# Kernel tuning notes

Measured on AMD Instinct MI355X. Metric: run time of the kernel, lower is better.

## Reference

```python
import jax, jax.numpy as jnp
import numpy as np

EPS = 1e-5

def conv3x3(x, w, b=None):
    # NCHW, OIHW, stride 1, padding 1
    y = jax.lax.conv_general_dilated(x, w, (1, 1), ((1, 1), (1, 1)),
                                     dimension_numbers=('NCHW', 'OIHW', 'NCHW'))
    if b is not None:
        y = y + b[None, :, None, None]
    return y

def batchnorm(x, g, b):
    # training-mode BN (PyTorch default): biased variance over (N,H,W)
    m = x.mean((0, 2, 3), keepdims=True)
    v = x.var((0, 2, 3), keepdims=True)
    return (x - m) * jax.lax.rsqrt(v + EPS) * g[None, :, None, None] + b[None, :, None, None]

def upsample2x_align_corners(x):
    # bilinear, align_corners=True, scale_factor=2
    def lerp_axis(a, Lin, axis):
        Lout = 2 * Lin
        c = jnp.arange(Lout, dtype=a.dtype) * (Lin - 1) / (Lout - 1)
        i0 = jnp.floor(c).astype(jnp.int32)
        i1 = jnp.minimum(i0 + 1, Lin - 1)
        w = c - i0.astype(a.dtype)
        shape = [1] * a.ndim
        shape[axis] = Lout
        w = w.reshape(shape)
        return jnp.take(a, i0, axis=axis) * (1 - w) + jnp.take(a, i1, axis=axis) * w
    x = lerp_axis(x, x.shape[2], 2)
    x = lerp_axis(x, x.shape[3], 3)
    return x

def deform_sample(x, offsets):
    # torchvision DeformConv2d v1 sampling: kernel 3x3, pad 1, offsets [B,18,H,W]
    # layout: per kernel point k (row-major), channels (2k, 2k+1) = (dy, dx)
    B, C, H, W = x.shape
    K = 9
    off = offsets.reshape(B, K, 2, H, W)
    ky, kx = jnp.meshgrid(jnp.arange(3) - 1, jnp.arange(3) - 1, indexing='ij')
    ky = ky.reshape(K).astype(x.dtype)
    kx = kx.reshape(K).astype(x.dtype)
    gy = jnp.arange(H, dtype=x.dtype)[None, None, :, None]
    gx = jnp.arange(W, dtype=x.dtype)[None, None, None, :]
    py = gy + ky[None, :, None, None] + off[:, :, 0]  # [B,K,H,W]
    px = gx + kx[None, :, None, None] + off[:, :, 1]
    y0 = jnp.floor(py)
    x0 = jnp.floor(px)
    wy = (py - y0)[:, None]  # [B,1,K,H,W]
    wx = (px - x0)[:, None]
    y0i = y0.astype(jnp.int32)
    x0i = x0.astype(jnp.int32)
    x_flat = x.reshape(B, C, H * W)
    def gather(yi, xi):
        valid = ((yi >= 0) & (yi < H) & (xi >= 0) & (xi < W))
        idx = jnp.clip(yi, 0, H - 1) * W + jnp.clip(xi, 0, W - 1)  # [B,K,H,W]
        g = jnp.take_along_axis(x_flat, idx.reshape(B, 1, K * H * W), axis=2)
        return g.reshape(B, C, K, H, W) * valid[:, None].astype(x.dtype)
    v00 = gather(y0i, x0i)
    v01 = gather(y0i, x0i + 1)
    v10 = gather(y0i + 1, x0i)
    v11 = gather(y0i + 1, x0i + 1)
    return (v00 * (1 - wy) * (1 - wx) + v01 * (1 - wy) * wx
            + v10 * wy * (1 - wx) + v11 * wy * wx)

def setup_inputs() -> dict:
    key = jax.random.key(0)
    ks = jax.random.split(key, 6)
    B, in_ch, skip_ch, out_ch = 4, 256, 128, 128
    Hs, Ws = 128, 128
    x = jax.random.normal(ks[0], (B, in_ch, Hs // 2, Ws // 2), jnp.float32)
    skip = jax.random.normal(ks[1], (B, skip_ch, Hs, Ws), jnp.float32)
    cat_ch = in_ch + skip_ch
    conv1_w = jax.random.normal(ks[2], (out_ch, cat_ch, 3, 3), jnp.float32) * (2.0 / (cat_ch * 9)) ** 0.5
    off_w = jax.random.normal(ks[3], (18, out_ch, 3, 3), jnp.float32) * 0.01
    off_b = jnp.zeros((18,), jnp.float32)
    def_w = jax.random.normal(ks[4], (out_ch, out_ch, 3, 3), jnp.float32) * (2.0 / (out_ch * 9)) ** 0.5
    def_b = jnp.zeros((out_ch,), jnp.float32)
    return {
        'x': x, 'skip': skip,
        'conv1_w': conv1_w,
        'bn1_g': jnp.ones((out_ch,), jnp.float32), 'bn1_b': jnp.zeros((out_ch,), jnp.float32),
        'off_w': off_w, 'off_b': off_b,
        'def_w': def_w, 'def_b': def_b,
        'bn2_g': jnp.ones((out_ch,), jnp.float32), 'bn2_b': jnp.zeros((out_ch,), jnp.float32),
    }

def reference(x, skip, conv1_w, bn1_g, bn1_b, off_w, off_b, def_w, def_b, bn2_g, bn2_b):
    xu = upsample2x_align_corners(x)
    dh = skip.shape[2] - xu.shape[2]
    dw = skip.shape[3] - xu.shape[3]
    if dh != 0 or dw != 0:
        xu = jnp.pad(xu, ((0, 0), (0, 0), (dh // 2, dh - dh // 2), (dw // 2, dw - dw // 2)))
    cat = jnp.concatenate([skip, xu], axis=1)
    h = jax.nn.relu(batchnorm(conv3x3(cat, conv1_w), bn1_g, bn1_b))
    offsets = conv3x3(h, off_w, off_b)  # [B,18,H,W]
    sampled = deform_sample(h, offsets)  # [B,C,9,H,W]
    O = def_w.shape[0]
    y = jnp.einsum('ock,bckhw->bohw', def_w.reshape(O, def_w.shape[1], 9), sampled)
    y = y + def_b[None, :, None, None]
    return jax.nn.relu(batchnorm(y, bn2_g, bn2_b))
```

## Files before the change

### kernel.cpp

```cpp
#include <hip/hip_runtime.h>
#include <hip/hip_bf16.h>

typedef __hip_bfloat16 bf16;
typedef __bf16 bf16x8 __attribute__((ext_vector_type(8)));
typedef __bf16 bf16x4 __attribute__((ext_vector_type(4)));
typedef float  f32x4  __attribute__((ext_vector_type(4)));

constexpr int NB   = 4;
constexpr int H    = 128;
constexpr int W    = 128;
constexpr int HW   = H * W;
constexpr int NPIX = NB * HW;
constexpr int CCAT = 384;
constexpr int CSKIP= 128;
constexpr int CIN  = 256;
constexpr int CO   = 128;
constexpr int HS   = 64;
constexpr int WP   = 130;
constexpr int K1   = 3456;
constexpr int KD   = 1152;
constexpr int NBORD= 2 * WP + 2 * (WP - 2);
constexpr float EPS = 1e-5f;

constexpr int NTR  = CO * K1 + 32 * KD + CO * KD;
constexpr int NCATB= NB * NBORD * CCAT;
constexpr int NHPB = NB * NBORD * CO;

__device__ __forceinline__ float b2f(bf16 v){ return __bfloat162float(v); }
__device__ __forceinline__ bf16  f2b(float v){ return __float2bfloat16(v); }

__device__ __forceinline__ void async_copy16(const void* g, void* s){
    __builtin_amdgcn_global_load_lds((const __attribute__((address_space(1))) void*)g,
                                     (__attribute__((address_space(3))) void*)s, 16, 0, 0);
}

__device__ __forceinline__ void border_yx(int p, int& y, int& x){
    if (p < WP)             { y = 0;        x = p; }
    else if (p < 2 * WP)    { y = WP - 1;   x = p - WP; }
    else if (p < 2 * WP + (WP - 2)) { y = p - 2 * WP + 1;          x = 0; }
    else                    { y = p - (2 * WP + (WP - 2)) + 1;     x = WP - 1; }
}

__global__ __launch_bounds__(256) void k_setup(const float* __restrict__ x,
                                               const float* __restrict__ skip,
                                               const float* __restrict__ w1,
                                               const float* __restrict__ wo,
                                               const float* __restrict__ wd,
                                               float* __restrict__ sums,
                                               bf16* __restrict__ catp,
                                               bf16* __restrict__ hp,
                                               bf16* __restrict__ wt1,
                                               bf16* __restrict__ wto,
                                               bf16* __restrict__ wtd){
    constexpr int TS = 66;
    __shared__ bf16 tile[128 * TS];
    int t = threadIdx.x;

    if (blockIdx.x < NB * H){
        int y  = blockIdx.x % H, b = blockIdx.x / H;
        int xx = t & 127, cp = t >> 7;

        float cy = (y * 63.0f) / 127.0f;
        int   y0 = (int)cy;
        int   y1 = min(y0 + 1, HS - 1);
        float wy = cy - y0;
        float cxf = (xx * 63.0f) / 127.0f;
        int   x0 = (int)cxf;
        int   x1 = min(x0 + 1, HS - 1);
        float wx = cxf - x0;

        bf16* orow = catp + (((size_t)b * WP + y + 1) * WP + 1) * CCAT;

        for (int chunk = 0; chunk < 6; chunk++){
            int cbase = chunk * 64;
            if (chunk >= 1) __syncthreads();
            if (chunk < 2){
                const float* sb = skip + ((size_t)(b * CSKIP + cbase + cp * 32) * H + y) * W;
#pragma unroll
                for (int i = 0; i < 32; i++)
                    tile[xx * TS + cp * 32 + i] = f2b(sb[(size_t)i * HW + xx]);
            } else {
                int icb = (chunk - 2) * 64 + cp * 32;
                const float* xr0 = x + ((size_t)(b * CIN + icb) * HS + y0) * HS;
                const float* xr1 = x + ((size_t)(b * CIN + icb) * HS + y1) * HS;
#pragma unroll
                for (int i = 0; i < 32; i++){
                    const float* r0 = xr0 + (size_t)i * HS * HS;
                    const float* r1 = xr1 + (size_t)i * HS * HS;
                    float v0 = r0[x0] * (1 - wx) + r0[x1] * wx;
                    float v1 = r1[x0] * (1 - wx) + r1[x1] * wx;
                    tile[xx * TS + cp * 32 + i] = f2b(v0 * (1 - wy) + v1 * wy);
                }
            }
            __syncthreads();
            int cc2 = (t & 31) * 2;
            int px0 = t >> 5;
#pragma unroll
            for (int pp = 0; pp < 16; pp++){
                int px = pp * 8 + px0;
                unsigned int v = *(const unsigned int*)&tile[px * TS + cc2];
                *(unsigned int*)&orow[(size_t)px * CCAT + cbase + cc2] = v;
            }
        }
        return;
    }

    int idx = (blockIdx.x - NB * H) * 256 + t;
    if (idx < NTR){
        int i = idx;
        if (i < CO * K1){
            int e  = i & 7;
            int l  = (i >> 3) & 63;
            int nb = (i >> 9) & 7;
            int ks = (i >> 12) & 1;
            int p  = i >> 13;
            int gp = p / 6, q = p - gp * 6;
            int ky = gp / 3, ci = gp - ky * 3;
            int kx = q >> 1, s64 = q & 1;
            int oc = nb * 16 + (l & 15);
            int ic = ci * 128 + s64 * 64 + ks * 32 + (l >> 4) * 8 + e;
            wt1[i] = f2b(w1[((oc * CCAT + ic) * 3 + ky) * 3 + kx]);
            return;
        }
        i -= CO * K1;
        if (i < 32 * KD){
            int e  = i & 7;
            int l  = (i >> 3) & 63;
            int wn = (i >> 9) & 1;
            int s  = (i >> 10) & 3;
            int kk = i >> 12;
            int ky = kk / 3, kx = kk - ky * 3;
            int oc = wn * 16 + (l & 15);
            int ic = s * 32 + (l >> 4) * 8 + e;
            wto[i] = (oc < 18) ? f2b(wo[((oc * CO + ic) * 3 + ky) * 3 + kx]) : f2b(0.f);
            return;
        }
        i -= 32 * KD;
        int e  = i & 7;
        int l  = (i >> 3) & 63;
        int ni = (i >> 9) & 3;
        int wn = (i >> 11) & 1;
        int ks = (i >> 12) & 1;
        int kc = i >> 13;
        int oc = wn * 64 + ni * 16 + (l & 15);
        int ic = (kc & 1) * 64 + ks * 32 + (l >> 4) * 8 + e;
        int kp = kc >> 1;
        wtd[i] = f2b(wd[(oc * CO + ic) * 9 + kp]);
        return;
    }
    idx -= NTR;
    if (idx < 512){ sums[idx] = 0.f; return; }
    idx -= 512;
    if (idx < NCATB){
        int c = idx % CCAT, r = idx / CCAT, p = r % NBORD, b = r / NBORD;
        int y, xw; border_yx(p, y, xw);
        catp[(((size_t)b * WP + y) * WP + xw) * CCAT + c] = f2b(0.f);
        return;
    }
    idx -= NCATB;
    if (idx < NHPB){
        int c = idx % CO, r = idx / CO, p = r % NBORD, b = r / NBORD;
        int y, xw; border_yx(p, y, xw);
        hp[(((size_t)b * WP + y) * WP + xw) * CO + c] = f2b(0.f);
    }
}

__global__ __launch_bounds__(256) void k_conv1_mfma(const bf16* __restrict__ catp,
                                                    const bf16* __restrict__ wbt,
                                                    bf16* __restrict__ hp,
                                                    float* __restrict__ sums){
    __shared__ unsigned short Ab[2][68 * 128];
    __shared__ float ps[256];
    int t = threadIdx.x;
    int l = t & 63, w = t >> 6;
    int half = blockIdx.x & 1;
    int y = (blockIdx.x >> 1) % H, b = blockIdx.x / (2 * H);
    int px0 = half * 64;

    int m = l & 15, quad = l >> 4;

    f32x4 acc[4][2];
#pragma unroll
    for (int i = 0; i < 4; i++)
#pragma unroll
        for (int j = 0; j < 2; j++) acc[i][j] = f32x4{0.f, 0.f, 0.f, 0.f};

    const size_t rowStride = (size_t)WP * CCAT;
    const char* wq = (const char*)wbt + w * 2048 + l * 16;

    bf16x8 bA[2][2], bB[2][2];

    {
        const bf16* Arow = catp + ((size_t)(b * WP) + y) * rowStride + (size_t)px0 * CCAT;
        for (int i = w; i < 17; i += 4){
            int G = i * 64 + l;
            int px = G >> 4, ol = G & 15;
            int osrc = ol ^ (px & 15);
            async_copy16(Arow + (size_t)px * CCAT + osrc * 8, &Ab[0][i * 512]);
        }
#pragma unroll
        for (int ks = 0; ks < 2; ks++)
#pragma unroll
            for (int ni = 0; ni < 2; ni++)
                bA[ks][ni] = *(const bf16x8*)(wq + ks * 8192 + ni * 1024);
    }
    __syncthreads();

#pragma unroll 1
    for (int g = 0; g < 9; g++){
        if (g < 8){
            int gn = g + 1;
            int kyn = gn / 3, cin = gn - kyn * 3;
            const bf16* Arow = catp + ((size_t)(b * WP) + y + kyn) * rowStride
                             + (size_t)px0 * CCAT + cin * 128;
            for (int i = w; i < 17; i += 4){
                int G = i * 64 + l;
                int px = G >> 4, ol = G & 15;
                int osrc = ol ^ (px & 15);
                async_copy16(Arow + (size_t)px * CCAT + osrc * 8, &Ab[gn & 1][i * 512]);
            }
        }
        const bf16x8* ap = (const bf16x8*)&Ab[g & 1][0];
        const char* wg = wq + (size_t)g * 6 * 16384;
#pragma unroll
        for (int j = 0; j < 6; j++){
            int kx = j >> 1, s64 = j & 1;
            const char* wnx = wg + (j + 1) * 16384;
            if (j & 1){
#pragma unroll
                for (int ks = 0; ks < 2; ks++)
#pragma unroll
                    for (int ni = 0; ni < 2; ni++)
                        bA[ks][ni] = *(const bf16x8*)(wnx + ks * 8192 + ni * 1024);
            } else {
#pragma unroll
                for (int ks = 0; ks < 2; ks++)
#pragma unroll
                    for (int ni = 0; ni < 2; ni++)
                        bB[ks][ni] = *(const bf16x8*)(wnx + ks * 8192 + ni * 1024);
            }
#pragma unroll
            for (int ks = 0; ks < 2; ks++){
                int s = s64 * 2 + ks;
                bf16x8 af[4];
#pragma unroll
                for (int mi = 0; mi < 4; mi++){
                    int pxk = mi * 16 + m + kx;
                    af[mi] = ap[pxk * 16 + ((s * 4 + quad) ^ (pxk & 15))];
                }
                if (j & 1){
#pragma unroll
                    for (int mi = 0; mi < 4; mi++)
#pragma unroll
                        for (int ni = 0; ni < 2; ni++)
                            acc[mi][ni] = __builtin_amdgcn_mfma_f32_16x16x32_bf16(
                                af[mi], bB[ks][ni], acc[mi][ni], 0, 0, 0);
                } else {
#pragma unroll
                    for (int mi = 0; mi < 4; mi++)
#pragma unroll
                        for (int ni = 0; ni < 2; ni++)
                            acc[mi][ni] = __builtin_amdgcn_mfma_f32_16x16x32_bf16(
                                af[mi], bA[ks][ni], acc[mi][ni], 0, 0, 0);
                }
            }
        }
        __syncthreads();
    }

    size_t obase = (((size_t)b * WP + y + 1) * WP + 1 + px0) * CO;
#pragma unroll
    for (int mi = 0; mi < 4; mi++){
        int p0 = mi * 16 + quad * 4;
#pragma unroll
        for (int ni = 0; ni < 2; ni++){
            int oc = w * 32 + ni * 16 + m;
#pragma unroll
            for (int r = 0; r < 4; r++)
                hp[obase + (size_t)(p0 + r) * CO + oc] = f2b(acc[mi][ni][r]);
        }
    }
    ps[t] = 0.f;
    __syncthreads();
#pragma unroll
    for (int ni = 0; ni < 2; ni++){
        int ch = w * 32 + ni * 16 + m;
        float s = 0.f, q2 = 0.f;
#pragma unroll
        for (int mi = 0; mi < 4; mi++)
#pragma unroll
            for (int r = 0; r < 4; r++){
                float v = acc[mi][ni][r];
                s += v; q2 += v * v;
            }
        s += __shfl_xor(s, 16); s += __shfl_xor(s, 32);
        q2 += __shfl_xor(q2, 16); q2 += __shfl_xor(q2, 32);
        if (quad == 0){
            atomicAdd(&ps[ch], s);
            atomicAdd(&ps[128 + ch], q2);
        }
    }
    __syncthreads();
    if (t < 128){
        atomicAdd(&sums[t],       ps[t]);
        atomicAdd(&sums[128 + t], ps[128 + t]);
    }
}

__global__ __launch_bounds__(256) void k_conv_off_mfma(const bf16* __restrict__ hp,
                                                       const bf16* __restrict__ wob,
                                                       const float* __restrict__ off_b,
                                                       const float* __restrict__ sums,
                                                       const float* __restrict__ bn_g,
                                                       const float* __restrict__ bn_b,
                                                       bf16* __restrict__ offs,
                                                       bf16* __restrict__ hq){
    __shared__ unsigned short Ab[68 * 128];
    __shared__ float2 ssc[128];
    int t = threadIdx.x, l = t & 63, w = t >> 6;
    if (t < 128){
        float mean = sums[t] / (float)NPIX;
        float var  = sums[128 + t] / (float)NPIX - mean * mean;
        float sc   = bn_g[t] * rsqrtf(var + EPS);
        ssc[t] = make_float2(sc, bn_b[t] - mean * sc);
    }
    int half = blockIdx.x & 1;
    int y = (blockIdx.x >> 1) % H, b = blockIdx.x / (2 * H);
    int px0 = half * 64;
    int m = l & 15, quad = l >> 4;
    int wm = w & 1, wn = w >> 1;

    f32x4 acc[2];
#pragma unroll
    for (int i = 0; i < 2; i++) acc[i] = f32x4{0.f, 0.f, 0.f, 0.f};

    const size_t rowStrideH = (size_t)WP * CO;
    const char* wq = (const char*)wob + wn * 1024 + l * 16;
    __syncthreads();

    for (int ky = 0; ky < 3; ky++){
        if (ky) __syncthreads();
        int row = y + ky;
        const bf16* Arow = hp + ((size_t)(b * WP) + row) * rowStrideH
                         + (size_t)px0 * CO;
        bool rowborder = (row == 0) || (row == WP - 1);
        bf16* hqrow = hq + ((size_t)(b * WP) + row) * rowStrideH;
        for (int i = w; i < 17; i += 4){
            int G  = i * 64 + l;
            int px = G >> 4, ol = G & 15;
            int osrc = ol ^ (px & 15);
            int col = px0 + px;
            bool zero = rowborder || (col == 0) || (col >= WP - 1);
            bf16x8 raw = *(const bf16x8*)(Arow + (size_t)px * CO + osrc * 8);
            bf16x8 outv;
#pragma unroll
            for (int e = 0; e < 8; e++){
                float2 sb = ssc[osrc * 8 + e];
                float v = (float)raw[e] * sb.x + sb.y;
                v = v > 0.f ? v : 0.f;
                outv[e] = zero ? (__bf16)0.f : (__bf16)v;
            }
            *(bf16x8*)&Ab[G * 8] = outv;
            if (ky == 1 && col >= 1 && col <= 128)
                *(bf16x8*)(hqrow + (size_t)col * CO + osrc * 8) = outv;
        }
        bf16x8 bfr[3][4];
#pragma unroll
        for (int kx = 0; kx < 3; kx++)
#pragma unroll
            for (int s = 0; s < 4; s++)
                bfr[kx][s] = *(const bf16x8*)(wq + (((ky * 3 + kx) * 4 + s) * 2048));
        __syncthreads();
        const bf16x8* ap = (const bf16x8*)Ab;
        for (int kx = 0; kx < 3; kx++){
#pragma unroll
            for (int s = 0; s < 4; s++){
#pragma unroll
                for (int mi = 0; mi < 2; mi++){
                    int pxk = wm * 32 + mi * 16 + m + kx;
                    bf16x8 af = ap[pxk * 16 + ((s * 4 + quad) ^ (pxk & 15))];
                    acc[mi] = __builtin_amdgcn_mfma_f32_16x16x32_bf16(af, bfr[kx][s], acc[mi], 0, 0, 0);
                }
            }
        }
    }
    int oc = wn * 16 + m;
    if (oc < 18){
        float bias = off_b[oc];
        int rowpix = b * HW + y * W + px0;
#pragma unroll
        for (int mi = 0; mi < 2; mi++){
            int p0 = wm * 32 + mi * 16 + quad * 4;
#pragma unroll
            for (int r = 0; r < 4; r++)
                offs[(size_t)(rowpix + p0 + r) * 18 + oc] = f2b(acc[mi][r] + bias);
        }
    }
}

__global__ __launch_bounds__(256) void k_deform_mfma(const bf16* __restrict__ hq,
                                                     const bf16* __restrict__ offs,
                                                     const bf16* __restrict__ wdb,
                                                     const float* __restrict__ def_b,
                                                     bf16* __restrict__ y,
                                                     float* __restrict__ sums){
    __shared__ unsigned short Ab[2][128 * 64];
    __shared__ int2   sc_yx[9 * 128];
    __shared__ float4 sc_w[9 * 128];
    __shared__ float  ps[256];

    int t = threadIdx.x, l = t & 63, w = t >> 6;
    int yrow = blockIdx.x % H, b = blockIdx.x / H;
    int rowpix = b * HW + yrow * W;

    for (int idx = t; idx < 9 * 128; idx += 256){
        int kp = idx >> 7, px = idx & 127;
        float dy = b2f(offs[(size_t)(rowpix + px) * 18 + 2 * kp]);
        float dx = b2f(offs[(size_t)(rowpix + px) * 18 + 2 * kp + 1]);
        float py = yrow + (kp / 3 - 1) + dy;
        float pxx = px + (kp % 3 - 1) + dx;
        float fy = floorf(py), fx = floorf(pxx);
        float wy = py - fy, wx = pxx - fx;
        int y0 = (int)fy, x0 = (int)fx;
        bool vy0 = (y0 >= 0) && (y0 < H);
        bool vy1 = (y0 + 1 >= 0) && (y0 + 1 < H);
        bool vx0 = (x0 >= 0) && (x0 < W);
        bool vx1 = (x0 + 1 >= 0) && (x0 + 1 < W);
        int y0c = min(max(y0, 0), H - 1),     y1c = min(max(y0 + 1, 0), H - 1);
        int x0c = min(max(x0, 0), W - 1),     x1c = min(max(x0 + 1, 0), W - 1);
        sc_yx[idx] = make_int2(((y0c + 1) * WP) | (((y1c + 1) * WP) << 16),
                               (x0c + 1) | ((x1c + 1) << 16));
        sc_w[idx] = make_float4((1 - wy) * (1 - wx) * (float)(vy0 && vx0),
                                (1 - wy) * wx       * (float)(vy0 && vx1),
                                wy * (1 - wx)       * (float)(vy1 && vx0),
                                wy * wx             * (float)(vy1 && vx1));
    }
    __syncthreads();

    int m = l & 15, quad = l >> 4;
    int wm = w & 1, wn = w >> 1;
    int g = l >> 4, j = l & 15;

    f32x4 acc[4][4];
#pragma unroll
    for (int i = 0; i < 4; i++)
#pragma unroll
        for (int jj = 0; jj < 4; jj++) acc[i][jj] = f32x4{0.f, 0.f, 0.f, 0.f};

    const bf16* hpb = hq + (size_t)b * WP * WP * CO;
    const char* wq = (const char*)wdb + wn * 4096 + l * 16;

    auto GEN = [&](int kc, unsigned short* dst){
        int kp = kc >> 1, ch = (kc & 1) * 64;
        int cb = ch + j * 4;
#pragma unroll
        for (int p = 0; p < 8; p++){
            int px = w * 32 + g * 8 + p;
            int idx = kp * 128 + px;
            int2 yx = sc_yx[idx];
            float4 w4 = sc_w[idx];
            int r0 = yx.x & 0xffff, r1 = ((unsigned)yx.x) >> 16;
            int c0 = yx.y & 0xffff, c1 = ((unsigned)yx.y) >> 16;
            const bf16* base = hpb + cb;
            bf16x4 s00 = *(const bf16x4*)(base + (size_t)(r0 + c0) * CO);
            bf16x4 s01 = *(const bf16x4*)(base + (size_t)(r0 + c1) * CO);
            bf16x4 s10 = *(const bf16x4*)(base + (size_t)(r1 + c0) * CO);
            bf16x4 s11 = *(const bf16x4*)(base + (size_t)(r1 + c1) * CO);
            bf16x4 pv;
#pragma unroll
            for (int r = 0; r < 4; r++){
                float v = w4.x * (float)s00[r] + w4.y * (float)s01[r]
                        + w4.z * (float)s10[r] + w4.w * (float)s11[r];
                pv[r] = (__bf16)v;
            }
            int oct_sw = (j >> 1) ^ (px & 7);
            *(bf16x4*)&dst[px * 64 + oct_sw * 8 + (j & 1) * 4] = pv;
        }
    };

    GEN(0, &Ab[0][0]);

#pragma unroll 1
    for (int kc = 0; kc < 18; kc++){
        __syncthreads();
        bf16x8 bfr[2][4];
        const char* wk = wq + (size_t)kc * 16384;
#pragma unroll
        for (int ks = 0; ks < 2; ks++)
#pragma unroll
            for (int ni = 0; ni < 4; ni++)
                bfr[ks][ni] = *(const bf16x8*)(wk + ks * 8192 + ni * 1024);
        if (kc < 17) GEN(kc + 1, &Ab[(kc + 1) & 1][0]);

        const bf16x8* ap = (const bf16x8*)&Ab[kc & 1][0];
#pragma unroll
        for (int ks = 0; ks < 2; ks++){
            bf16x8 af[4];
#pragma unroll
            for (int mi = 0; mi < 4; mi++){
                int px = wm * 64 + mi * 16 + m;
                af[mi] = ap[px * 8 + ((ks * 4 + quad) ^ (px & 7))];
            }
#pragma unroll
            for (int mi = 0; mi < 4; mi++)
#pragma unroll
                for (int ni = 0; ni < 4; ni++)
                    acc[mi][ni] = __builtin_amdgcn_mfma_f32_16x16x32_bf16(
                        af[mi], bfr[ks][ni], acc[mi][ni], 0, 0, 0);
        }
    }
#pragma unroll
    for (int mi = 0; mi < 4; mi++){
        int p0 = wm * 64 + mi * 16 + quad * 4;
#pragma unroll
        for (int ni = 0; ni < 4; ni++){
            int oc = wn * 64 + ni * 16 + m;
            float bias = def_b[oc];
#pragma unroll
            for (int r = 0; r < 4; r++)
                y[(size_t)(rowpix + p0 + r) * CO + oc] = f2b(acc[mi][ni][r] + bias);
        }
    }
    ps[t] = 0.f;
    __syncthreads();
#pragma unroll
    for (int ni = 0; ni < 4; ni++){
        int ch = wn * 64 + ni * 16 + m;
        float bias = def_b[ch];
        float s = 0.f, q = 0.f;
#pragma unroll
        for (int mi = 0; mi < 4; mi++)
#pragma unroll
            for (int r = 0; r < 4; r++){
                float v = acc[mi][ni][r] + bias;
                s += v; q += v * v;
            }
        s += __shfl_xor(s, 16); s += __shfl_xor(s, 32);
        q += __shfl_xor(q, 16); q += __shfl_xor(q, 32);
        if (quad == 0){
            atomicAdd(&ps[ch], s);
            atomicAdd(&ps[128 + ch], q);
        }
    }
    __syncthreads();
    if (t < 128){
        atomicAdd(&sums[t],       ps[t]);
        atomicAdd(&sums[128 + t], ps[128 + t]);
    }
}

__global__ __launch_bounds__(256) void k_final(const bf16* __restrict__ yb,
                                               const float* __restrict__ sums,
                                               const float* __restrict__ g,
                                               const float* __restrict__ bb,
                                               float* __restrict__ out){
    __shared__ unsigned short tile[128 * 129];
    __shared__ float ssc[256];
    int t = threadIdx.x;
    if (t < 128){
        float mean = sums[t] / (float)NPIX;
        float var  = sums[128 + t] / (float)NPIX - mean * mean;
        float scale = g[t] * rsqrtf(var + EPS);
        ssc[t]       = scale;
        ssc[128 + t] = bb[t] - mean * scale;
    }
    int yrow = blockIdx.x % H, b = blockIdx.x / H;
    int rowbase = b * HW + yrow * W;
    const unsigned short* src = (const unsigned short*)yb;
    for (int it = 0; it < 64; it++){
        int idx = it * 256 + t;
        int c = idx & 127, px = idx >> 7;
        tile[px * 129 + c] = src[(size_t)(rowbase + px) * CO + c];
    }
    __syncthreads();
    for (int it = 0; it < 64; it++){
        int idx = it * 256 + t;
        int xw = idx & 127, o = idx >> 7;
        unsigned short u = tile[xw * 129 + o];
        float v = (float)(*(const __bf16*)&u);
        v = v * ssc[o] + ssc[128 + o];
        out[(((size_t)b * CO + o) * H + yrow) * W + xw] = v > 0.f ? v : 0.f;
    }
}

extern "C" void kernel_launch(void* const* d_in, const int* in_sizes, int n_in,
                              void* d_out, int out_size, void* d_ws, size_t ws_size,
                              hipStream_t stream){
    const float* x      = (const float*)d_in[0];
    const float* skip   = (const float*)d_in[1];
    const float* conv1w = (const float*)d_in[2];
    const float* bn1g   = (const float*)d_in[3];
    const float* bn1b   = (const float*)d_in[4];
    const float* offw   = (const float*)d_in[5];
    const float* offb   = (const float*)d_in[6];
    const float* defw   = (const float*)d_in[7];
    const float* defb   = (const float*)d_in[8];
    const float* bn2g   = (const float*)d_in[9];
    const float* bn2b   = (const float*)d_in[10];
    float* out = (float*)d_out;

    char* ws = (char*)d_ws;
    size_t off_bytes = 0;
    auto alloc = [&](size_t bytes) -> void* {
        void* p = ws + off_bytes;
        off_bytes += (bytes + 255) & ~(size_t)255;
        return p;
    };
    const size_t catp_elems = (size_t)NB * WP * WP * CCAT;
    const size_t hp_elems   = (size_t)NB * WP * WP * CO;
    bf16*  catp  = (bf16*) alloc(catp_elems * 2 + 2048);
    bf16*  hp    = (bf16*) alloc(hp_elems * 2 + 2048);
    bf16*  hq    = (bf16*) alloc(hp_elems * 2 + 2048);
    bf16*  offs  = (bf16*) alloc((size_t)NPIX * 18 * 2);
    bf16*  yb    = (bf16*) alloc((size_t)NPIX * CO * 2);
    bf16*  wbt   = (bf16*) alloc((size_t)CO * K1 * 2 + 32768);
    bf16*  wob   = (bf16*) alloc((size_t)32 * KD * 2);
    bf16*  wdb   = (bf16*) alloc((size_t)CO * KD * 2);
    float* sums  = (float*)alloc(512 * 4);
    float* sums1 = sums;
    float* sums2 = sums + 256;

    const int nflat = NTR + 512 + NCATB + NHPB;
    const int setup_blocks = NB * H + (nflat + 255) / 256;

    k_setup<<<setup_blocks, 256, 0, stream>>>(x, skip, conv1w, offw, defw,
                                              sums, catp, hp, wbt, wob, wdb);

    k_conv1_mfma<<<NB * H * 2, 256, 0, stream>>>(catp, wbt, hp, sums1);

    k_conv_off_mfma<<<NB * H * 2, 256, 0, stream>>>(hp, wob, offb, sums1,
                                                    bn1g, bn1b, offs, hq);

    k_deform_mfma<<<NB * H, 256, 0, stream>>>(hq, offs, wdb, defb, yb, sums2);

    k_final<<<NB * H, 256, 0, stream>>>(yb, sums2, bn2g, bn2b, out);
}
```

Baseline: 314.5 us.

## Fuse all stages into one persistent kernel with software grid barriers

Replaces the five separate kernel launches (setup, conv1, offset conv, deformable conv, final BN) with a single persistent kernel of 256 blocks that grid-strides over row tiles and separates the stages with atomic-counter grid barriers. The aim is to remove per-launch overhead and the idle gaps between dependent kernels. In exchange the grid is limited to 256 blocks with launch bounds of 1, which lowers occupancy and the parallelism of the MFMA stages. Correctness also depends on every block being co-resident and on the spin barrier behaving correctly.

```diff
diff --git a/kernel.cpp b/kernel.cpp
--- a/kernel.cpp
+++ b/kernel.cpp
@@ -25,6 +25,9 @@
 constexpr int NTR  = CO * K1 + 32 * KD + CO * KD;
 constexpr int NCATB= NB * NBORD * CCAT;
 constexpr int NHPB = NB * NBORD * CO;
+constexpr int NFLAT= NTR + 512 + NCATB + NHPB;
+
+constexpr int GRID = 256;
 
 __device__ __forceinline__ float b2f(bf16 v){ return __bfloat162float(v); }
 __device__ __forceinline__ bf16  f2b(float v){ return __float2bfloat16(v); }
@@ -41,33 +44,49 @@
     else                    { y = p - (2 * WP + (WP - 2)) + 1;     x = WP - 1; }
 }
 
-__global__ __launch_bounds__(256) void k_setup(const float* __restrict__ x,
-                                               const float* __restrict__ skip,
-                                               const float* __restrict__ w1,
-                                               const float* __restrict__ wo,
-                                               const float* __restrict__ wd,
-                                               float* __restrict__ sums,
-                                               bf16* __restrict__ catp,
-                                               bf16* __restrict__ hp,
-                                               bf16* __restrict__ wt1,
-                                               bf16* __restrict__ wto,
-                                               bf16* __restrict__ wtd){
-    constexpr int TS = 66;
-    __shared__ bf16 tile[128 * TS];
+__device__ __forceinline__ void gsync(unsigned* bar, unsigned target){
+    __syncthreads();
+    if (threadIdx.x == 0){
+        __threadfence();
+        atomicAdd(bar, 1u);
+        while (atomicAdd(bar, 0u) < target)
+            __builtin_amdgcn_s_sleep(8);
+        __threadfence();
+    }
+    __syncthreads();
+}
+
+__global__ void __launch_bounds__(256, 1) k_fused(
+    const float* __restrict__ x,    const float* __restrict__ skip,
+    const float* __restrict__ w1,   const float* __restrict__ bn1g,
+    const float* __restrict__ bn1b, const float* __restrict__ wo,
+    const float* __restrict__ offb, const float* __restrict__ wd,
+    const float* __restrict__ defb, const float* __restrict__ bn2g,
+    const float* __restrict__ bn2b, float* __restrict__ out,
+    bf16* __restrict__ catp, bf16* __restrict__ hp, bf16* __restrict__ hq,
+    bf16* __restrict__ offs, bf16* __restrict__ yb,
+    bf16* __restrict__ wt1, bf16* __restrict__ wto, bf16* __restrict__ wtd,
+    float* __restrict__ sums, unsigned* __restrict__ bar)
+{
+    __shared__ __align__(16) char smem[61440];
     int t = threadIdx.x;
-
-    if (blockIdx.x < NB * H){
-        int y  = blockIdx.x % H, b = blockIdx.x / H;
+    float* sums1 = sums;
+    float* sums2 = sums + 256;
+
+    for (int vb = blockIdx.x; vb < 512; vb += GRID){
+        constexpr int TS = 66;
+        bf16* tile = (bf16*)smem;
+        int y  = vb % H, b = vb / H;
         int xx = t & 127, cp = t >> 7;
 
         float cy = (y * 63.0f) / 127.0f;
         int   y0 = (int)cy;
         int   y1 = min(y0 + 1, HS - 1);
-        float wy = cy - y0;
+        float wyf = cy - y0;
         float cxf = (xx * 63.0f) / 127.0f;
         int   x0 = (int)cxf;
         int   x1 = min(x0 + 1, HS - 1);
-        float wx = cxf - x0;
+        float wxf = cxf - x0;
 
         bf16* orow = catp + (((size_t)b * WP + y + 1) * WP + 1) * CCAT;
 
@@ -87,9 +106,9 @@
                 for (int i = 0; i < 32; i++){
                     const float* r0 = xr0 + (size_t)i * HS * HS;
                     const float* r1 = xr1 + (size_t)i * HS * HS;
-                    float v0 = r0[x0] * (1 - wx) + r0[x1] * wx;
-                    float v1 = r1[x0] * (1 - wx) + r1[x1] * wx;
-                    tile[xx * TS + cp * 32 + i] = f2b(v0 * (1 - wy) + v1 * wy);
+                    float v0 = r0[x0] * (1 - wxf) + r0[x1] * wxf;
+                    float v1 = r1[x0] * (1 - wxf) + r1[x1] * wxf;
+                    tile[xx * TS + cp * 32 + i] = f2b(v0 * (1 - wyf) + v1 * wyf);
                 }
             }
             __syncthreads();
@@ -102,11 +121,9 @@
                 *(unsigned int*)&orow[(size_t)px * CCAT + cbase + cc2] = v;
             }
         }
-        return;
+        __syncthreads();
     }
-
-    int idx = (blockIdx.x - NB * H) * 256 + t;
-    if (idx < NTR){
+    for (int idx = blockIdx.x * 256 + t; idx < NFLAT; idx += GRID * 256){
         int i = idx;
         if (i < CO * K1){
             int e  = i & 7;
@@ -120,7 +137,7 @@
             int oc = nb * 16 + (l & 15);
             int ic = ci * 128 + s64 * 64 + ks * 32 + (l >> 4) * 8 + e;
             wt1[i] = f2b(w1[((oc * CCAT + ic) * 3 + ky) * 3 + kx]);
-            return;
+            continue;
         }
         i -= CO * K1;
         if (i < 32 * KD){
@@ -133,453 +150,446 @@
             int oc = wn * 16 + (l & 15);
             int ic = s * 32 + (l >> 4) * 8 + e;
             wto[i] = (oc < 18) ? f2b(wo[((oc * CO + ic) * 3 + ky) * 3 + kx]) : f2b(0.f);
-            return;
+            continue;
         }
         i -= 32 * KD;
-        int e  = i & 7;
-        int l  = (i >> 3) & 63;
-        int ni = (i >> 9) & 3;
-        int wn = (i >> 11) & 1;
-        int ks = (i >> 12) & 1;
-        int kc = i >> 13;
-        int oc = wn * 64 + ni * 16 + (l & 15);
-        int ic = (kc & 1) * 64 + ks * 32 + (l >> 4) * 8 + e;
-        int kp = kc >> 1;
-        wtd[i] = f2b(wd[(oc * CO + ic) * 9 + kp]);
-        return;
+        if (i < CO * KD){
+            int e  = i & 7;
+            int l  = (i >> 3) & 63;
+            int ni = (i >> 9) & 3;
+            int wn = (i >> 11) & 1;
+            int ks = (i >> 12) & 1;
+            int kc = i >> 13;
+            int oc = wn * 64 + ni * 16 + (l & 15);
+            int ic = (kc & 1) * 64 + ks * 32 + (l >> 4) * 8 + e;
+            int kp = kc >> 1;
+            wtd[i] = f2b(wd[(oc * CO + ic) * 9 + kp]);
+            continue;
+        }
+        i -= CO * KD;
+        if (i < 512){ sums[i] = 0.f; continue; }
+        i -= 512;
+        if (i < NCATB){
+            int c = i % CCAT, r = i / CCAT, p = r % NBORD, b2 = r / NBORD;
+            int yy, xw; border_yx(p, yy, xw);
+            catp[(((size_t)b2 * WP + yy) * WP + xw) * CCAT + c] = f2b(0.f);
+            continue;
+        }
+        i -= NCATB;
+        {
+            int c = i % CO, r = i / CO, p = r % NBORD, b2 = r / NBORD;
+            int yy, xw; border_yx(p, yy, xw);
+            hp[(((size_t)b2 * WP + yy) * WP + xw) * CO + c] = f2b(0.f);
+        }
     }
-    idx -= NTR;
-    if (idx < 512){ sums[idx] = 0.f; return; }
-    idx -= 512;
-    if (idx < NCATB){
-        int c = idx % CCAT, r = idx / CCAT, p = r % NBORD, b = r / NBORD;
-        int y, xw; border_yx(p, y, xw);
-        catp[(((size_t)b * WP + y) * WP + xw) * CCAT + c] = f2b(0.f);
-        return;
+    gsync(bar, GRID * 1);
+
+    for (int vb = blockIdx.x; vb < 512; vb += GRID){
+        typedef unsigned short AbT[68 * 128];
+        AbT* Ab = (AbT*)smem;
+        float* ps = (float*)(smem + 34816);
+        int l = t & 63, w = t >> 6;
+        int y = vb % H, b = vb / H;
+        int m = l & 15, quad = l >> 4;
+        const size_t rowStride = (size_t)WP * CCAT;
+        const char* wq = (const char*)wt1 + w * 2048 + l * 16;
+
+        for (int u = 0; u < 2; u++){
+            int px0 = u * 64;
+            f32x4 acc[4][2];
+#pragma unroll
+            for (int i = 0; i < 4; i++)
+#pragma unroll
+                for (int j = 0; j < 2; j++) acc[i][j] = f32x4{0.f, 0.f, 0.f, 0.f};
+
+            bf16x8 bA[2][2], bB[2][2];
+            {
+                const bf16* Arow = catp + ((size_t)(b * WP) + y) * rowStride + (size_t)px0 * CCAT;
+                for (int i = w; i < 17; i += 4){
+                    int G = i * 64 + l;
+                    int px = G >> 4, ol = G & 15;
+                    int osrc = ol ^ (px & 15);
+                    async_copy16(Arow + (size_t)px * CCAT + osrc * 8, &Ab[0][i * 512]);
+                }
+#pragma unroll
+                for (int ks = 0; ks < 2; ks++)
+#pragma unroll
+                    for (int ni = 0; ni < 2; ni++)
+                        bA[ks][ni] = *(const bf16x8*)(wq + ks * 8192 + ni * 1024);
+            }
+            __syncthreads();
+
+#pragma unroll 1
+            for (int g = 0; g < 9; g++){
+                if (g < 8){
+                    int gn = g + 1;
+                    int kyn = gn / 3, cin = gn - kyn * 3;
+                    const bf16* Arow = catp + ((size_t)(b * WP) + y + kyn) * rowStride
+                                     + (size_t)px0 * CCAT + cin * 128;
+                    for (int i = w; i < 17; i += 4){
+                        int G = i * 64 + l;
+                        int px = G >> 4, ol = G & 15;
+                        int osrc = ol ^ (px & 15);
+                        async_copy16(Arow + (size_t)px * CCAT + osrc * 8, &Ab[gn & 1][i * 512]);
+                    }
+                }
+                const bf16x8* ap = (const bf16x8*)&Ab[g & 1][0];
+                const char* wg = wq + (size_t)g * 6 * 16384;
+#pragma unroll
+                for (int j = 0; j < 6; j++){
+                    int kx = j >> 1, s64 = j & 1;
+                    const char* wnx = wg + (j + 1) * 16384;
+                    if (j & 1){
+#pragma unroll
+                        for (int ks = 0; ks < 2; ks++)
+#pragma unroll
+                            for (int ni = 0; ni < 2; ni++)
+                                bA[ks][ni] = *(const bf16x8*)(wnx + ks * 8192 + ni * 1024);
+                    } else {
+#pragma unroll
+                        for (int ks = 0; ks < 2; ks++)
+#pragma unroll
+                            for (int ni = 0; ni < 2; ni++)
+                                bB[ks][ni] = *(const bf16x8*)(wnx + ks * 8192 + ni * 1024);
+                    }
+#pragma unroll
+                    for (int ks = 0; ks < 2; ks++){
+                        int s = s64 * 2 + ks;
+                        bf16x8 af[4];
+#pragma unroll
+                        for (int mi = 0; mi < 4; mi++){
+                            int pxk = mi * 16 + m + kx;
+                            af[mi] = ap[pxk * 16 + ((s * 4 + quad) ^ (pxk & 15))];
+                        }
+                        if (j & 1){
+#pragma unroll
+                            for (int mi = 0; mi < 4; mi++)
+#pragma unroll
+                                for (int ni = 0; ni < 2; ni++)
+                                    acc[mi][ni] = __builtin_amdgcn_mfma_f32_16x16x32_bf16(
+                                        af[mi], bB[ks][ni], acc[mi][ni], 0, 0, 0);
+                        } else {
+#pragma unroll
+                            for (int mi = 0; mi < 4; mi++)
+#pragma unroll
+                                for (int ni = 0; ni < 2; ni++)
+                                    acc[mi][ni] = __builtin_amdgcn_mfma_f32_16x16x32_bf16(
+                                        af[mi], bA[ks][ni], acc[mi][ni], 0, 0, 0);
+                        }
+                    }
+                }
+                __syncthreads();
+            }
+
+            size_t obase = (((size_t)b * WP + y + 1) * WP + 1 + px0) * CO;
+#pragma unroll
+            for (int mi = 0; mi < 4; mi++){
+                int p0 = mi * 16 + quad * 4;
+#pragma unroll
+                for (int ni = 0; ni < 2; ni++){
+                    int oc = w * 32 + ni * 16 + m;
+#pragma unroll
+                    for (int r = 0; r < 4; r++)
+                        hp[obase + (size_t)(p0 + r) * CO + oc] = f2b(acc[mi][ni][r]);
+                }
+            }
+            ps[t] = 0.f;
+            __syncthreads();
+#pragma unroll
+            for (int ni = 0; ni < 2; ni++){
+                int ch = w * 32 + ni * 16 + m;
+                float s = 0.f, q2 = 0.f;
+#pragma unroll
+                for (int mi = 0; mi < 4; mi++)
+#pragma unroll
+                    for (int r = 0; r < 4; r++){
+                        float v = acc[mi][ni][r];
+                        s += v; q2 += v * v;
+                    }
+                s += __shfl_xor(s, 16); s += __shfl_xor(s, 32);
+                q2 += __shfl_xor(q2, 16); q2 += __shfl_xor(q2, 32);
+                if (quad == 0){
+                    atomicAdd(&ps[ch], s);
+                    atomicAdd(&ps[128 + ch], q2);
+                }
+            }
+            __syncthreads();
+            if (t < 128){
+                atomicAdd(&sums1[t],       ps[t]);
+                atomicAdd(&sums1[128 + t], ps[128 + t]);
+            }
+            __syncthreads();
+        }
     }
-    idx -= NCATB;
-    if (idx < NHPB){
-        int c = idx % CO, r = idx / CO, p = r % NBORD, b = r / NBORD;
-        int y, xw; border_yx(p, y, xw);
-        hp[(((size_t)b * WP + y) * WP + xw) * CO + c] = f2b(0.f);
+    gsync(bar, GRID * 2);
+
+    {
+        unsigned short* Ab = (unsigned short*)smem;
+        float2* ssc = (float2*)(smem + 17408);
+        int l = t & 63, w = t >> 6;
+        if (t < 128){
+            float mean = sums1[t] / (float)NPIX;
+            float var  = sums1[128 + t] / (float)NPIX - mean * mean;
+            float sc   = bn1g[t] * rsqrtf(var + EPS);
+            ssc[t] = make_float2(sc, bn1b[t] - mean * sc);
+        }
+        int m = l & 15, quad = l >> 4;
+        int wm = w & 1, wn = w >> 1;
+        const size_t rowStrideH = (size_t)WP * CO;
+        const char* wq = (const char*)wto + wn * 1024 + l * 16;
+        __syncthreads();
+
+        for (int vb = blockIdx.x; vb < 512; vb += GRID){
+            int y = vb % H, b = vb / H;
+            for (int u = 0; u < 2; u++){
+                int px0 = u * 64;
+                f32x4 acc[2];
+#pragma unroll
+                for (int i = 0; i < 2; i++) acc[i] = f32x4{0.f, 0.f, 0.f, 0.f};
+
+                for (int ky = 0; ky < 3; ky++){
+                    __syncthreads();
+                    int row = y + ky;
+                    const bf16* Arow = hp + ((size_t)(b * WP) + row) * rowStrideH
+                                     + (size_t)px0 * CO;
+                    bool rowborder = (row == 0) || (row == WP - 1);
+                    bf16* hqrow = hq + ((size_t)(b * WP) + row) * rowStrideH;
+                    for (int i = w; i < 17; i += 4){
+                        int G  = i * 64 + l;
+                        int px = G >> 4, ol = G & 15;
+                        int osrc = ol ^ (px & 15);
+                        int col = px0 + px;
+                        bool zero = rowborder || (col == 0) || (col >= WP - 1);
+                        bf16x8 raw = *(const bf16x8*)(Arow + (size_t)px * CO + osrc * 8);
+                        bf16x8 outv;
+#pragma unroll
+                        for (int e = 0; e < 8; e++){
+                            float2 sb = ssc[osrc * 8 + e];
+                            float v = (float)raw[e] * sb.x + sb.y;
+                            v = v > 0.f ? v : 0.f;
+                            outv[e] = zero ? (__bf16)0.f : (__bf16)v;
+                        }
+                        *(bf16x8*)&Ab[G * 8] = outv;
+                        if (ky == 1 && col >= 1 && col <= 128)
+                            *(bf16x8*)(hqrow + (size_t)col * CO + osrc * 8) = outv;
+                    }
+                    bf16x8 bfr[3][4];
+#pragma unroll
+                    for (int kx = 0; kx < 3; kx++)
+#pragma unroll
+                        for (int s = 0; s < 4; s++)
+                            bfr[kx][s] = *(const bf16x8*)(wq + (((ky * 3 + kx) * 4 + s) * 2048));
+                    __syncthreads();
+                    const bf16x8* ap = (const bf16x8*)Ab;
+                    for (int kx = 0; kx < 3; kx++){
+#pragma unroll
+                        for (int s = 0; s < 4; s++){
+#pragma unroll
+                            for (int mi = 0; mi < 2; mi++){
+                                int pxk = wm * 32 + mi * 16 + m + kx;
+                                bf16x8 af = ap[pxk * 16 + ((s * 4 + quad) ^ (pxk & 15))];
+                                acc[mi] = __builtin_amdgcn_mfma_f32_16x16x32_bf16(af, bfr[kx][s], acc[mi], 0, 0, 0);
+                            }
+                        }
+                    }
+                }
+                int oc = wn * 16 + m;
+                if (oc < 18){
+                    float bias = offb[oc];
+                    int rowpix = b * HW + y * W + px0;
+#pragma unroll
+                    for (int mi = 0; mi < 2; mi++){
+                        int p0 = wm * 32 + mi * 16 + quad * 4;
+#pragma unroll
+                        for (int r = 0; r < 4; r++)
+                            offs[(size_t)(rowpix + p0 + r) * 18 + oc] = f2b(acc[mi][r] + bias);
+                    }
+                }
+                __syncthreads();
+            }
+        }
     }
-}
-
-__global__ __launch_bounds__(256) void k_conv1_mfma(const bf16* __restrict__ catp,
-                                                    const bf16* __restrict__ wbt,
-                                                    bf16* __restrict__ hp,
-                                                    float* __restrict__ sums){
-    __shared__ unsigned short Ab[2][68 * 128];
-    __shared__ float ps[256];
-    int t = threadIdx.x;
-    int l = t & 63, w = t >> 6;
-    int half = blockIdx.x & 1;
-    int y = (blockIdx.x >> 1) % H, b = blockIdx.x / (2 * H);
-    int px0 = half * 64;
-
-    int m = l & 15, quad = l >> 4;
-
-    f32x4 acc[4][2];
-#pragma unroll
-    for (int i = 0; i < 4; i++)
-#pragma unroll
-        for (int j = 0; j < 2; j++) acc[i][j] = f32x4{0.f, 0.f, 0.f, 0.f};
-
-    const size_t rowStride = (size_t)WP * CCAT;
-    const char* wq = (const char*)wbt + w * 2048 + l * 16;
-
-    bf16x8 bA[2][2], bB[2][2];
-
-    {
-        const bf16* Arow = catp + ((size_t)(b * WP) + y) * rowStride + (size_t)px0 * CCAT;
-        for (int i = w; i < 17; i += 4){
-            int G = i * 64 + l;
-            int px = G >> 4, ol = G & 15;
-            int osrc = ol ^ (px & 15);
-            async_copy16(Arow + (size_t)px * CCAT + osrc * 8, &Ab[0][i * 512]);
-        }
-#pragma unroll
-        for (int ks = 0; ks < 2; ks++)
-#pragma unroll
-            for (int ni = 0; ni < 2; ni++)
-                bA[ks][ni] = *(const bf16x8*)(wq + ks * 8192 + ni * 1024);
-    }
-    __syncthreads();
+    gsync(bar, GRID * 3);
+
+    for (int vb = blockIdx.x; vb < 512; vb += GRID){
+        typedef unsigned short AbT[128 * 64];
+        AbT* Ab = (AbT*)smem;
+        int2*   sc_yx = (int2*)(smem + 32768);
+        float4* sc_w  = (float4*)(smem + 41984);
+        float*  ps    = (float*)(smem + 60416);
+        int l = t & 63, w = t >> 6;
+        int yrow = vb % H, b = vb / H;
+        int rowpix = b * HW + yrow * W;
+
+        for (int idx = t; idx < 9 * 128; idx += 256){
+            int kp = idx >> 7, px = idx & 127;
+            float dy = b2f(offs[(size_t)(rowpix + px) * 18 + 2 * kp]);
+            float dx = b2f(offs[(size_t)(rowpix + px) * 18 + 2 * kp + 1]);
+            float py = yrow + (kp / 3 - 1) + dy;
+            float pxx = px + (kp % 3 - 1) + dx;
+            float fy = floorf(py), fx = floorf(pxx);
+            float wy = py - fy, wx = pxx - fx;
+            int y0 = (int)fy, x0 = (int)fx;
+            bool vy0 = (y0 >= 0) && (y0 < H);
+            bool vy1 = (y0 + 1 >= 0) && (y0 + 1 < H);
+            bool vx0 = (x0 >= 0) && (x0 < W);
+            bool vx1 = (x0 + 1 >= 0) && (x0 + 1 < W);
+            int y0c = min(max(y0, 0), H - 1),     y1c = min(max(y0 + 1, 0), H - 1);
+            int x0c = min(max(x0, 0), W - 1),     x1c = min(max(x0 + 1, 0), W - 1);
+            sc_yx[idx] = make_int2(((y0c + 1) * WP) | (((y1c + 1) * WP) << 16),
+                                   (x0c + 1) | ((x1c + 1) << 16));
+            sc_w[idx] = make_float4((1 - wy) * (1 - wx) * (float)(vy0 && vx0),
+                                    (1 - wy) * wx       * (float)(vy0 && vx1),
+                                    wy * (1 - wx)       * (float)(vy1 && vx0),
+                                    wy * wx             * (float)(vy1 && vx1));
+        }
+        __syncthreads();
+
+        int m = l & 15, quad = l >> 4;
+        int wm = w & 1, wn = w >> 1;
+        int g = l >> 4, j = l & 15;
+
+        f32x4 acc[4][4];
+#pragma unroll
+        for (int i = 0; i < 4; i++)
+#pragma unroll
+            for (int jj = 0; jj < 4; jj++) acc[i][jj] = f32x4{0.f, 0.f, 0.f, 0.f};
+
+        const bf16* hpb = hq + (size_t)b * WP * WP * CO;
+        const char* wq = (const char*)wtd + wn * 4096 + l * 16;
+
+        auto GEN = [&](int kc, unsigned short* dst){
+            int kp = kc >> 1, ch = (kc & 1) * 64;
+            int cb = ch + j * 4;
+#pragma unroll
+            for (int p = 0; p < 8; p++){
+                int px = w * 32 + g * 8 + p;
+                int idx = kp * 128 + px;
+                int2 yx = sc_yx[idx];
+                float4 w4 = sc_w[idx];
+                int r0 = yx.x & 0xffff, r1 = ((unsigned)yx.x) >> 16;
+                int c0 = yx.y & 0xffff, c1 = ((unsigned)yx.y) >> 16;
+                const bf16* base = hpb + cb;
+                bf16x4 s00 = *(const bf16x4*)(base + (size_t)(r0 + c0) * CO);
+                bf16x4 s01 = *(const bf16x4*)(base + (size_t)(r0 + c1) * CO);
+                bf16x4 s10 = *(const bf16x4*)(base + (size_t)(r1 + c0) * CO);
+                bf16x4 s11 = *(const bf16x4*)(base + (size_t)(r1 + c1) * CO);
+                bf16x4 pv;
+#pragma unroll
+                for (int r = 0; r < 4; r++){
+                    float v = w4.x * (float)s00[r] + w4.y * (float)s01[r]
+                            + w4.z * (float)s10[r] + w4.w * (float)s11[r];
+                    pv[r] = (__bf16)v;
+                }
+                int oct_sw = (j >> 1) ^ (px & 7);
+                *(bf16x4*)&dst[px * 64 + oct_sw * 8 + (j & 1) * 4] = pv;
+            }
+        };
+
+        GEN(0, &Ab[0][0]);
 
 #pragma unroll 1
-    for (int g = 0; g < 9; g++){
-        if (g < 8){
-            int gn = g + 1;
-            int kyn = gn / 3, cin = gn - kyn * 3;
-            const bf16* Arow = catp + ((size_t)(b * WP) + y + kyn) * rowStride
-                             + (size_t)px0 * CCAT + cin * 128;
-            for (int i = w; i < 17; i += 4){
-                int G = i * 64 + l;
-                int px = G >> 4, ol = G & 15;
-                int osrc = ol ^ (px & 15);
-                async_copy16(Arow + (size_t)px * CCAT + osrc * 8, &Ab[gn & 1][i * 512]);
-            }
-        }
-        const bf16x8* ap = (const bf16x8*)&Ab[g & 1][0];
-        const char* wg = wq + (size_t)g * 6 * 16384;
-#pragma unroll
-        for (int j = 0; j < 6; j++){
-            int kx = j >> 1, s64 = j & 1;
-            const char* wnx = wg + (j + 1) * 16384;
-            if (j & 1){
-#pragma unroll
-                for (int ks = 0; ks < 2; ks++)
-#pragma unroll
-                    for (int ni = 0; ni < 2; ni++)
-                        bA[ks][ni] = *(const bf16x8*)(wnx + ks * 8192 + ni * 1024);
-            } else {
-#pragma unroll
-                for (int ks = 0; ks < 2; ks++)
-#pragma unroll
-                    for (int ni = 0; ni < 2; ni++)
-                        bB[ks][ni] = *(const bf16x8*)(wnx + ks * 8192 + ni * 1024);
-            }
+        for (int kc = 0; kc < 18; kc++){
+            __syncthreads();
+            bf16x8 bfr[2][4];
+            const char* wk = wq + (size_t)kc * 16384;
+#pragma unroll
+            for (int ks = 0; ks < 2; ks++)
+#pragma unroll
+                for (int ni = 0; ni < 4; ni++)
+                    bfr[ks][ni] = *(const bf16x8*)(wk + ks * 8192 + ni * 1024);
+            if (kc < 17) GEN(kc + 1, &Ab[(kc + 1) & 1][0]);
+
+            const bf16x8* ap = (const bf16x8*)&Ab[kc & 1][0];
 #pragma unroll
             for (int ks = 0; ks < 2; ks++){
-                int s = s64 * 2 + ks;
                 bf16x8 af[4];
 #pragma unroll
                 for (int mi = 0; mi < 4; mi++){
-                    int pxk = mi * 16 + m + kx;
-                    af[mi] = ap[pxk * 16 + ((s * 4 + quad) ^ (pxk & 15))];
-                }
-                if (j & 1){
-#pragma unroll
-                    for (int mi = 0; mi < 4; mi++)
-#pragma unroll
-                        for (int ni = 0; ni < 2; ni++)
-                            acc[mi][ni] = __builtin_amdgcn_mfma_f32_16x16x32_bf16(
-                                af[mi], bB[ks][ni], acc[mi][ni], 0, 0, 0);
-                } else {
-#pragma unroll
-                    for (int mi = 0; mi < 4; mi++)
-#pragma unroll
-                        for (int ni = 0; ni < 2; ni++)
-                            acc[mi][ni] = __builtin_amdgcn_mfma_f32_16x16x32_bf16(
-                                af[mi], bA[ks][ni], acc[mi][ni], 0, 0, 0);
-                }
-            }
+                    int px = wm * 64 + mi * 16 + m;
+                    af[mi] = ap[px * 8 + ((ks * 4 + quad) ^ (px & 7))];
+                }
+#pragma unroll
+                for (int mi = 0; mi < 4; mi++)
+#pragma unroll
+                    for (int ni = 0; ni < 4; ni++)
+                        acc[mi][ni] = __builtin_amdgcn_mfma_f32_16x16x32_bf16(
+                            af[mi], bfr[ks][ni], acc[mi][ni], 0, 0, 0);
+            }
+        }
+#pragma unroll
+        for (int mi = 0; mi < 4; mi++){
+            int p0 = wm * 64 + mi * 16 + quad * 4;
+#pragma unroll
+            for (int ni = 0; ni < 4; ni++){
+                int oc = wn * 64 + ni * 16 + m;
+                float bias = defb[oc];
+#pragma unroll
+                for (int r = 0; r < 4; r++)
+                    yb[(size_t)(rowpix + p0 + r) * CO + oc] = f2b(acc[mi][ni][r] + bias);
+            }
+        }
+        ps[t] = 0.f;
+        __syncthreads();
+#pragma unroll
+        for (int ni = 0; ni < 4; ni++){
+            int ch = wn * 64 + ni * 16 + m;
+            float bias = defb[ch];
+            float s = 0.f, q = 0.f;
+#pragma unroll
+            for (int mi = 0; mi < 4; mi++)
+#pragma unroll
+                for (int r = 0; r < 4; r++){
+                    float v = acc[mi][ni][r] + bias;
+                    s += v; q += v * v;
+                }
+            s += __shfl_xor(s, 16); s += __shfl_xor(s, 32);
+            q += __shfl_xor(q, 16); q += __shfl_xor(q, 32);
+            if (quad == 0){
+                atomicAdd(&ps[ch], s);
+                atomicAdd(&ps[128 + ch], q);
+            }
+        }
+        __syncthreads();
+        if (t < 128){
+            atomicAdd(&sums2[t],       ps[t]);
+            atomicAdd(&sums2[128 + t], ps[128 + t]);
         }
         __syncthreads();
     }
-
-    size_t obase = (((size_t)b * WP + y + 1) * WP + 1 + px0) * CO;
-#pragma unroll
-    for (int mi = 0; mi < 4; mi++){
-        int p0 = mi * 16 + quad * 4;
-#pragma unroll
-        for (int ni = 0; ni < 2; ni++){
-            int oc = w * 32 + ni * 16 + m;
-#pragma unroll
-            for (int r = 0; r < 4; r++)
-                hp[obase + (size_t)(p0 + r) * CO + oc] = f2b(acc[mi][ni][r]);
-        }
-    }
-    ps[t] = 0.f;
-    __syncthreads();
-#pragma unroll
-    for (int ni = 0; ni < 2; ni++){
-        int ch = w * 32 + ni * 16 + m;
-        float s = 0.f, q2 = 0.f;
-#pragma unroll
-        for (int mi = 0; mi < 4; mi++)
-#pragma unroll
-            for (int r = 0; r < 4; r++){
-                float v = acc[mi][ni][r];
-                s += v; q2 += v * v;
-            }
-        s += __shfl_xor(s, 16); s += __shfl_xor(s, 32);
-        q2 += __shfl_xor(q2, 16); q2 += __shfl_xor(q2, 32);
-        if (quad == 0){
-            atomicAdd(&ps[ch], s);
-            atomicAdd(&ps[128 + ch], q2);
-        }
-    }
-    __syncthreads();
-    if (t < 128){
-        atomicAdd(&sums[t],       ps[t]);
-        atomicAdd(&sums[128 + t], ps[128 + t]);
-    }
-}
-
-__global__ __launch_bounds__(256) void k_conv_off_mfma(const bf16* __restrict__ hp,
-                                                       const bf16* __restrict__ wob,
-                                                       const float* __restrict__ off_b,
-                                                       const float* __restrict__ sums,
-                                                       const float* __restrict__ bn_g,
-                                                       const float* __restrict__ bn_b,
-                                                       bf16* __restrict__ offs,
-                                                       bf16* __restrict__ hq){
-    __shared__ unsigned short Ab[68 * 128];
-    __shared__ float2 ssc[128];
-    int t = threadIdx.x, l = t & 63, w = t >> 6;
-    if (t < 128){
-        float mean = sums[t] / (float)NPIX;
-        float var  = sums[128 + t] / (float)NPIX - mean * mean;
-        float sc   = bn_g[t] * rsqrtf(var + EPS);
-        ssc[t] = make_float2(sc, bn_b[t] - mean * sc);
-    }
-    int half = blockIdx.x & 1;
-    int y = (blockIdx.x >> 1) % H, b = blockIdx.x / (2 * H);
-    int px0 = half * 64;
-    int m = l & 15, quad = l >> 4;
-    int wm = w & 1, wn = w >> 1;
-
-    f32x4 acc[2];
-#pragma unroll
-    for (int i = 0; i < 2; i++) acc[i] = f32x4{0.f, 0.f, 0.f, 0.f};
-
-    const size_t rowStrideH = (size_t)WP * CO;
-    const char* wq = (const char*)wob + wn * 1024 + l * 16;
-    __syncthreads();
-
-    for (int ky = 0; ky < 3; ky++){
-        if (ky) __syncthreads();
-        int row = y + ky;
-        const bf16* Arow = hp + ((size_t)(b * WP) + row) * rowStrideH
-                         + (size_t)px0 * CO;
-        bool rowborder = (row == 0) || (row == WP - 1);
-        bf16* hqrow = hq + ((size_t)(b * WP) + row) * rowStrideH;
-        for (int i = w; i < 17; i += 4){
-            int G  = i * 64 + l;
-            int px = G >> 4, ol = G & 15;
-            int osrc = ol ^ (px & 15);
-            int col = px0 + px;
-            bool zero = rowborder || (col == 0) || (col >= WP - 1);
-            bf16x8 raw = *(const bf16x8*)(Arow + (size_t)px * CO + osrc * 8);
-            bf16x8 outv;
-#pragma unroll
-            for (int e = 0; e < 8; e++){
-                float2 sb = ssc[osrc * 8 + e];
-                float v = (float)raw[e] * sb.x + sb.y;
-                v = v > 0.f ? v : 0.f;
-                outv[e] = zero ? (__bf16)0.f : (__bf16)v;
-            }
-            *(bf16x8*)&Ab[G * 8] = outv;
-            if (ky == 1 && col >= 1 && col <= 128)
-                *(bf16x8*)(hqrow + (size_t)col * CO + osrc * 8) = outv;
-        }
-        bf16x8 bfr[3][4];
-#pragma unroll
-        for (int kx = 0; kx < 3; kx++)
-#pragma unroll
-            for (int s = 0; s < 4; s++)
-                bfr[kx][s] = *(const bf16x8*)(wq + (((ky * 3 + kx) * 4 + s) * 2048));
+    gsync(bar, GRID * 4);
+
+    {
+        unsigned short* tile = (unsigned short*)smem;
+        float* ssc = (float*)(smem + 33024);
+        if (t < 128){
+            float mean = sums2[t] / (float)NPIX;
+            float var  = sums2[128 + t] / (float)NPIX - mean * mean;
+            float scale = bn2g[t] * rsqrtf(var + EPS);
+            ssc[t]       = scale;
+            ssc[128 + t] = bn2b[t] - mean * scale;
+        }
         __syncthreads();
-        const bf16x8* ap = (const bf16x8*)Ab;
-        for (int kx = 0; kx < 3; kx++){
-#pragma unroll
-            for (int s = 0; s < 4; s++){
-#pragma unroll
-                for (int mi = 0; mi < 2; mi++){
-                    int pxk = wm * 32 + mi * 16 + m + kx;
-                    bf16x8 af = ap[pxk * 16 + ((s * 4 + quad) ^ (pxk & 15))];
-                    acc[mi] = __builtin_amdgcn_mfma_f32_16x16x32_bf16(af, bfr[kx][s], acc[mi], 0, 0, 0);
-                }
-            }
-        }
-    }
-    int oc = wn * 16 + m;
-    if (oc < 18){
-        float bias = off_b[oc];
-        int rowpix = b * HW + y * W + px0;
-#pragma unroll
-        for (int mi = 0; mi < 2; mi++){
-            int p0 = wm * 32 + mi * 16 + quad * 4;
-#pragma unroll
-            for (int r = 0; r < 4; r++)
-                offs[(size_t)(rowpix + p0 + r) * 18 + oc] = f2b(acc[mi][r] + bias);
-        }
-    }
-}
-
-__global__ __launch_bounds__(256) void k_deform_mfma(const bf16* __restrict__ hq,
-                                                     const bf16* __restrict__ offs,
-                                                     const bf16* __restrict__ wdb,
-                                                     const float* __restrict__ def_b,
-                                                     bf16* __restrict__ y,
-                                                     float* __restrict__ sums){
-    __shared__ unsigned short Ab[2][128 * 64];
-    __shared__ int2   sc_yx[9 * 128];
-    __shared__ float4 sc_w[9 * 128];
-    __shared__ float  ps[256];
-
-    int t = threadIdx.x, l = t & 63, w = t >> 6;
-    int yrow = blockIdx.x % H, b = blockIdx.x / H;
-    int rowpix = b * HW + yrow * W;
-
-    for (int idx = t; idx < 9 * 128; idx += 256){
-        int kp = idx >> 7, px = idx & 127;
-        float dy = b2f(offs[(size_t)(rowpix + px) * 18 + 2 * kp]);
-        float dx = b2f(offs[(size_t)(rowpix + px) * 18 + 2 * kp + 1]);
-        float py = yrow + (kp / 3 - 1) + dy;
-        float pxx = px + (kp % 3 - 1) + dx;
-        float fy = floorf(py), fx = floorf(pxx);
-        float wy = py - fy, wx = pxx - fx;
-        int y0 = (int)fy, x0 = (int)fx;
-        bool vy0 = (y0 >= 0) && (y0 < H);
-        bool vy1 = (y0 + 1 >= 0) && (y0 + 1 < H);
-        bool vx0 = (x0 >= 0) && (x0 < W);
-        bool vx1 = (x0 + 1 >= 0) && (x0 + 1 < W);
-        int y0c = min(max(y0, 0), H - 1),     y1c = min(max(y0 + 1, 0), H - 1);
-        int x0c = min(max(x0, 0), W - 1),     x1c = min(max(x0 + 1, 0), W - 1);
-        sc_yx[idx] = make_int2(((y0c + 1) * WP) | (((y1c + 1) * WP) << 16),
-                               (x0c + 1) | ((x1c + 1) << 16));
-        sc_w[idx] = make_float4((1 - wy) * (1 - wx) * (float)(vy0 && vx0),
-                                (1 - wy) * wx       * (float)(vy0 && vx1),
-                                wy * (1 - wx)       * (float)(vy1 && vx0),
-                                wy * wx             * (float)(vy1 && vx1));
-    }
-    __syncthreads();
-
-    int m = l & 15, quad = l >> 4;
-    int wm = w & 1, wn = w >> 1;
-    int g = l >> 4, j = l & 15;
-
-    f32x4 acc[4][4];
-#pragma unroll
-    for (int i = 0; i < 4; i++)
-#pragma unroll
-        for (int jj = 0; jj < 4; jj++) acc[i][jj] = f32x4{0.f, 0.f, 0.f, 0.f};
-
-    const bf16* hpb = hq + (size_t)b * WP * WP * CO;
-    const char* wq = (const char*)wdb + wn * 4096 + l * 16;
-
-    auto GEN = [&](int kc, unsigned short* dst){
-        int kp = kc >> 1, ch = (kc & 1) * 64;
-        int cb = ch + j * 4;
-#pragma unroll
-        for (int p = 0; p < 8; p++){
-            int px = w * 32 + g * 8 + p;
-            int idx = kp * 128 + px;
-            int2 yx = sc_yx[idx];
-            float4 w4 = sc_w[idx];
-            int r0 = yx.x & 0xffff, r1 = ((unsigned)yx.x) >> 16;
-            int c0 = yx.y & 0xffff, c1 = ((unsigned)yx.y) >> 16;
-            const bf16* base = hpb + cb;
-            bf16x4 s00 = *(const bf16x4*)(base + (size_t)(r0 + c0) * CO);
-            bf16x4 s01 = *(const bf16x4*)(base + (size_t)(r0 + c1) * CO);
-            bf16x4 s10 = *(const bf16x4*)(base + (size_t)(r1 + c0) * CO);
-            bf16x4 s11 = *(const bf16x4*)(base + (size_t)(r1 + c1) * CO);
-            bf16x4 pv;
-#pragma unroll
-            for (int r = 0; r < 4; r++){
-                float v = w4.x * (float)s00[r] + w4.y * (float)s01[r]
-                        + w4.z * (float)s10[r] + w4.w * (float)s11[r];
-                pv[r] = (__bf16)v;
-            }
-            int oct_sw = (j >> 1) ^ (px & 7);
-            *(bf16x4*)&dst[px * 64 + oct_sw * 8 + (j & 1) * 4] = pv;
-        }
-    };
-
-    GEN(0, &Ab[0][0]);
-
-#pragma unroll 1
-    for (int kc = 0; kc < 18; kc++){
-        __syncthreads();
-        bf16x8 bfr[2][4];
-        const char* wk = wq + (size_t)kc * 16384;
-#pragma unroll
-        for (int ks = 0; ks < 2; ks++)
-#pragma unroll
-            for (int ni = 0; ni < 4; ni++)
-                bfr[ks][ni] = *(const bf16x8*)(wk + ks * 8192 + ni * 1024);
-        if (kc < 17) GEN(kc + 1, &Ab[(kc + 1) & 1][0]);
-
-        const bf16x8* ap = (const bf16x8*)&Ab[kc & 1][0];
-#pragma unroll
-        for (int ks = 0; ks < 2; ks++){
-            bf16x8 af[4];
-#pragma unroll
-            for (int mi = 0; mi < 4; mi++){
-                int px = wm * 64 + mi * 16 + m;
-                af[mi] = ap[px * 8 + ((ks * 4 + quad) ^ (px & 7))];
-            }
-#pragma unroll
-            for (int mi = 0; mi < 4; mi++)
-#pragma unroll
-                for (int ni = 0; ni < 4; ni++)
-                    acc[mi][ni] = __builtin_amdgcn_mfma_f32_16x16x32_bf16(
-                        af[mi], bfr[ks][ni], acc[mi][ni], 0, 0, 0);
-        }
-    }
-#pragma unroll
-    for (int mi = 0; mi < 4; mi++){
-        int p0 = wm * 64 + mi * 16 + quad * 4;
-#pragma unroll
-        for (int ni = 0; ni < 4; ni++){
-            int oc = wn * 64 + ni * 16 + m;
-            float bias = def_b[oc];
-#pragma unroll
-            for (int r = 0; r < 4; r++)
-                y[(size_t)(rowpix + p0 + r) * CO + oc] = f2b(acc[mi][ni][r] + bias);
-        }
-    }
-    ps[t] = 0.f;
-    __syncthreads();
-#pragma unroll
-    for (int ni = 0; ni < 4; ni++){
-        int ch = wn * 64 + ni * 16 + m;
-        float bias = def_b[ch];
-        float s = 0.f, q = 0.f;
-#pragma unroll
-        for (int mi = 0; mi < 4; mi++)
-#pragma unroll
-            for (int r = 0; r < 4; r++){
-                float v = acc[mi][ni][r] + bias;
-                s += v; q += v * v;
-            }
-        s += __shfl_xor(s, 16); s += __shfl_xor(s, 32);
-        q += __shfl_xor(q, 16); q += __shfl_xor(q, 32);
-        if (quad == 0){
-            atomicAdd(&ps[ch], s);
-            atomicAdd(&ps[128 + ch], q);
-        }
-    }
-    __syncthreads();
-    if (t < 128){
-        atomicAdd(&sums[t],       ps[t]);
-        atomicAdd(&sums[128 + t], ps[128 + t]);
-    }
-}
-
-__global__ __launch_bounds__(256) void k_final(const bf16* __restrict__ yb,
-                                               const float* __restrict__ sums,
-                                               const float* __restrict__ g,
-                                               const float* __restrict__ bb,
-                                               float* __restrict__ out){
-    __shared__ unsigned short tile[128 * 129];
-    __shared__ float ssc[256];
-    int t = threadIdx.x;
-    if (t < 128){
-        float mean = sums[t] / (float)NPIX;
-        float var  = sums[128 + t] / (float)NPIX - mean * mean;
-        float scale = g[t] * rsqrtf(var + EPS);
-        ssc[t]       = scale;
-        ssc[128 + t] = bb[t] - mean * scale;
-    }
-    int yrow = blockIdx.x % H, b = blockIdx.x / H;
-    int rowbase = b * HW + yrow * W;
-    const unsigned short* src = (const unsigned short*)yb;
-    for (int it = 0; it < 64; it++){
-        int idx = it * 256 + t;
-        int c = idx & 127, px = idx >> 7;
-        tile[px * 129 + c] = src[(size_t)(rowbase + px) * CO + c];
-    }
-    __syncthreads();
-    for (int it = 0; it < 64; it++){
-        int idx = it * 256 + t;
-        int xw = idx & 127, o = idx >> 7;
-        unsigned short u = tile[xw * 129 + o];
-        float v = (float)(*(const __bf16*)&u);
-        v = v * ssc[o] + ssc[128 + o];
-        out[(((size_t)b * CO + o) * H + yrow) * W + xw] = v > 0.f ? v : 0.f;
+        const unsigned short* src = (const unsigned short*)yb;
+        for (int vb = blockIdx.x; vb < 512; vb += GRID){
+            int yrow = vb % H, b = vb / H;
+            int rowbase = b * HW + yrow * W;
+            for (int it = 0; it < 64; it++){
+                int idx = it * 256 + t;
+                int c = idx & 127, px = idx >> 7;
+                tile[px * 129 + c] = src[(size_t)(rowbase + px) * CO + c];
+            }
+            __syncthreads();
+            for (int it = 0; it < 64; it++){
+                int idx = it * 256 + t;
+                int xw = idx & 127, o = idx >> 7;
+                unsigned short u = tile[xw * 129 + o];
+                float v = (float)(*(const __bf16*)&u);
+                v = v * ssc[o] + ssc[128 + o];
+                out[(((size_t)b * CO + o) * H + yrow) * W + xw] = v > 0.f ? v : 0.f;
+            }
+            __syncthreads();
+        }
     }
 }
 
@@ -617,21 +627,12 @@
     bf16*  wob   = (bf16*) alloc((size_t)32 * KD * 2);
     bf16*  wdb   = (bf16*) alloc((size_t)CO * KD * 2);
     float* sums  = (float*)alloc(512 * 4);
-    float* sums1 = sums;
-    float* sums2 = sums + 256;
-
-    const int nflat = NTR + 512 + NCATB + NHPB;
-    const int setup_blocks = NB * H + (nflat + 255) / 256;
-
-    k_setup<<<setup_blocks, 256, 0, stream>>>(x, skip, conv1w, offw, defw,
-                                              sums, catp, hp, wbt, wob, wdb);
-
-    k_conv1_mfma<<<NB * H * 2, 256, 0, stream>>>(catp, wbt, hp, sums1);
-
-    k_conv_off_mfma<<<NB * H * 2, 256, 0, stream>>>(hp, wob, offb, sums1,
-                                                    bn1g, bn1b, offs, hq);
-
-    k_deform_mfma<<<NB * H, 256, 0, stream>>>(hq, offs, wdb, defb, yb, sums2);
-
-    k_final<<<NB * H, 256, 0, stream>>>(yb, sums2, bn2g, bn2b, out);
+    unsigned* bar = (unsigned*)alloc(256);
+
+    hipMemsetAsync(bar, 0, 256, stream);
+
+    k_fused<<<GRID, 256, 0, stream>>>(x, skip, conv1w, bn1g, bn1b,
+                                      offw, offb, defw, defb, bn2g, bn2b, out,
+                                      catp, hp, hq, offs, yb,
+                                      wbt, wob, wdb, sums, bar);
 }
```

After: 555.5 us. 76.7% more time.
